# Performance work log

Hardware: AMD Instinct MI355X
Metric: run time of the kernel (lower is better)

Reference implementation:

```python
import jax, jax.numpy as jnp
import numpy as np

NLOC = 10  # local nodes per element (cubic DG triangle)


def setup_inputs() -> dict:
    key = jax.random.key(0)
    ks = jax.random.split(key, 6)
    nele, nloc, ngi = 500000, NLOC, 13
    return {
        "r0": jax.random.normal(ks[0], (nele * nloc,), dtype=jnp.float32),
        "c_i": jax.random.normal(ks[1], (nele * nloc,), dtype=jnp.float32),
        "c_n": jax.random.normal(ks[2], (nele, 1, nloc), dtype=jnp.float32),
        "k": jnp.ones((1,), dtype=jnp.float32),
        "dt": jnp.ones((1,), dtype=jnp.float32),
        "n": jax.random.normal(ks[3], (nloc, ngi), dtype=jnp.float32),
        "nx": jax.random.normal(ks[4], (nele, 2, nloc, ngi), dtype=jnp.float32),
        "detwei": jax.random.uniform(ks[5], (nele, ngi), dtype=jnp.float32),
    }


def reference(r0, c_i, c_n, k, dt, n, nx, detwei):
    nele, _, nloc, ngi = nx.shape
    c_i = c_i.reshape(nele, 1, nloc)               # [e,1,l]
    # stiffness: sum over spatial dims of grad-grad quadrature contraction
    nx1nx1 = jnp.einsum('eig,ejg,eg->eij', nx[:, 0], nx[:, 0], detwei)
    nx2nx2 = jnp.einsum('eig,ejg,eg->eij', nx[:, 1], nx[:, 1], detwei)
    nxnx = (nx1nx1 + nx2nx2) * k                   # [e,i,j] * [1]
    # mass matrix per element (shared shape funcs, per-element detwei)
    nn = jnp.einsum('ig,jg,eg->eij', n, n, detwei)
    # transient branch (config.isTransient = True)
    nn_dt = nn / dt
    nxnx = nn_dt + nxnx
    r0 = r0.reshape(nele, nloc, 1)
    r0 = r0 + jnp.matmul(nn_dt, jnp.swapaxes(c_n, 1, 2))   # [e,i,1]
    r0 = r0.reshape(-1)
    r0 = r0 - jnp.matmul(nxnx, jnp.swapaxes(c_i, 1, 2)).reshape(-1)
    diagA = jnp.diagonal(nxnx, axis1=-2, axis2=-1)          # [e,nloc]
    bdiagA = nxnx
    return (bdiagA, diagA, r0)
```

## Files before the change

### kernel.cpp

```cpp
#include <hip/hip_runtime.h>

#define NLOC  10
#define NGI   13
#define NPAIR 55
#define EPB   32
#define TPB   128

#define B_NX   0
#define B_DW   8320
#define B_R0   8736
#define B_CI   9056
#define B_CN   9376
#define BUF_FL 9696
#define W_N    (2 * BUF_FL)
#define W_TOT  (W_N + 130)

#define GE_NX  2080
#define GE_DW  2184
#define GE_R0  2264
#define GE_CI  2344
#define GE_CN  2424

typedef float vf2 __attribute__((ext_vector_type(2)));

__device__ __forceinline__ constexpr int pidx(int i, int j) {
    return i * NLOC - (i * (i - 1)) / 2 + (j - i);
}

__device__ __forceinline__ void stage16(const float* gsrc, float* lds) {
    __builtin_amdgcn_global_load_lds(
        (const __attribute__((address_space(1))) void*)gsrc,
        (__attribute__((address_space(3))) void*)lds, 16, 0, 0);
}

__global__ __launch_bounds__(TPB, 1) void fem_kernel(
    const float* __restrict__ r0g,
    const float* __restrict__ cig,
    const float* __restrict__ cng,
    const float* __restrict__ kp,
    const float* __restrict__ dtp,
    const float* __restrict__ nmat,
    const float* __restrict__ nx,
    const float* __restrict__ dwei,
    float* __restrict__ out,
    int nele)
{
    __shared__ float sm[W_TOT];

    const int t       = threadIdx.x;
    const int nchunks = (nele + EPB - 1) / EPB;
    const int gs      = gridDim.x;

    auto stage_chunk = [&](int b, int c) {
        const long ce0  = (long)c * EPB;
        const int  crem = min(EPB, nele - (int)ce0);
        const float* snx = nx   + (size_t)ce0 * 260;
        const float* sdw = dwei + (size_t)ce0 * 13;
        const float* sr0 = r0g  + (size_t)ce0 * 10;
        const float* sci = cig  + (size_t)ce0 * 10;
        const float* scn = cng  + (size_t)ce0 * 10;
        const int cnx = crem * 260, cdw = crem * 13, c10 = crem * 10;
        float* ldsb = sm + b * BUF_FL + (t >> 6) * 256;
        #pragma unroll
        for (int k = 0; k < 19; ++k) {
            const int G = k * TPB + t;
            const float* src; int rel, capf;
            if      (G < GE_NX) { src = snx; rel = G;         capf = cnx; }
            else if (G < GE_DW) { src = sdw; rel = G - GE_NX; capf = cdw; }
            else if (G < GE_R0) { src = sr0; rel = G - GE_DW; capf = c10; }
            else if (G < GE_CI) { src = sci; rel = G - GE_R0; capf = c10; }
            else if (G < GE_CN) { src = scn; rel = G - GE_CI; capf = c10; }
            else continue;
            if (rel * 4 < capf) stage16(src + (size_t)rel * 4, ldsb + k * TPB * 4);
        }
    };

    const int  eloc = t >> 2;
    const int  d    = (t >> 1) & 1;
    const int  h    = t & 1;
    const int  q    = t & 3;
    const float kk  = kp[0];
    const float idt = 1.0f / dtp[0];
    const float* smn = sm + W_N;

    int c = blockIdx.x;
    if (c < nchunks) stage_chunk(0, c);
    for (int w = t; w < 130; w += TPB) sm[W_N + w] = nmat[w];
    __syncthreads();

    int cur = 0;
    for (; c < nchunks; c += gs) {
        const int next = c + gs;
        if (next < nchunks) stage_chunk(cur ^ 1, next);

        const long e0   = (long)c * EPB;
        const int  rem  = min(EPB, nele - (int)e0);
        const long e    = e0 + eloc;
        const bool live = eloc < rem;

        const float* bb   = sm + cur * BUF_FL;
        const float* smnx = bb + B_NX + eloc * 260 + d * 130;
        const float* smdw = bb + B_DW + eloc * 13;
        const float* smr0 = bb + B_R0 + eloc * 10;
        const float* smci = bb + B_CI + eloc * 10;
        const float* smcn = bb + B_CN + eloc * 10;

        float civ[NLOC], dif[NLOC];
        #pragma unroll
        for (int l = 0; l < NLOC; ++l) civ[l] = smci[l];
        #pragma unroll
        for (int l = 0; l < NLOC; ++l) dif[l] = smcn[l] - civ[l];

        float acc[NPAIR];
        #pragma unroll
        for (int p = 0; p < NPAIR; ++p) acc[p] = 0.0f;
        float r0a[NLOC];
        #pragma unroll
        for (int i = 0; i < NLOC; ++i) r0a[i] = 0.0f;

        #pragma unroll
        for (int it = 0; it < 7; ++it) {
            const int   graw = 2 * it + h;
            const int   g    = graw < NGI ? graw : NGI - 1;
            const float wv   = graw < NGI ? kk * smdw[g] : 0.0f;
            float col[NLOC];
            #pragma unroll
            for (int l = 0; l < NLOC; ++l) col[l] = smnx[l * 13 + g];
            float u = 0.0f;
            #pragma unroll
            for (int l = 0; l < NLOC; ++l) u = fmaf(col[l], civ[l], u);
            const float uw = u * wv;
            #pragma unroll
            for (int i = 0; i < NLOC; ++i) {
                const float ti = col[i] * wv;
                #pragma unroll
                for (int j = i; j < NLOC; ++j)
                    acc[pidx(i, j)] = fmaf(ti, col[j], acc[pidx(i, j)]);
                r0a[i] = fmaf(-col[i], uw, r0a[i]);
            }
        }

        #pragma unroll
        for (int it = 0; it < 4; ++it) {
            const int   graw = q + 4 * it;
            const int   g    = graw < NGI ? graw : NGI - 1;
            const float wv   = graw < NGI ? idt * smdw[g] : 0.0f;
            float ncol[NLOC];
            #pragma unroll
            for (int l = 0; l < NLOC; ++l) ncol[l] = smn[l * 13 + g];
            float wd = 0.0f;
            #pragma unroll
            for (int l = 0; l < NLOC; ++l) wd = fmaf(ncol[l], dif[l], wd);
            #pragma unroll
            for (int i = 0; i < NLOC; ++i) {
                const float ti = ncol[i] * wv;
                #pragma unroll
                for (int j = i; j < NLOC; ++j)
                    acc[pidx(i, j)] = fmaf(ti, ncol[j], acc[pidx(i, j)]);
                r0a[i] = fmaf(ti, wd, r0a[i]);
            }
        }

        #pragma unroll
        for (int p = 0; p < NPAIR; ++p) {
            acc[p] += __shfl_xor(acc[p], 1);
            acc[p] += __shfl_xor(acc[p], 2);
        }
        #pragma unroll
        for (int i = 0; i < NLOC; ++i) {
            r0a[i] += __shfl_xor(r0a[i], 1);
            r0a[i] += __shfl_xor(r0a[i], 2);
        }

        if (live) {
            float* obd = out + (size_t)e * 100;
            float* odg = out + (size_t)nele * 100 + (size_t)e * 10;
            float* oro = out + (size_t)nele * 110 + (size_t)e * 10;
            #pragma unroll
            for (int i = 0; i < NLOC; ++i) {
                if ((i & 3) == q) {
                    float row[NLOC];
                    #pragma unroll
                    for (int j = 0; j < NLOC; ++j) {
                        const int lo = i < j ? i : j, hi = i < j ? j : i;
                        row[j] = acc[pidx(lo, hi)];
                    }
                    #pragma unroll
                    for (int u2 = 0; u2 < 5; ++u2) {
                        vf2 v = { row[2*u2], row[2*u2+1] };
                        *reinterpret_cast<vf2*>(obd + i * 10 + 2 * u2) = v;
                    }
                    odg[i] = row[i];
                    oro[i] = smr0[i] + r0a[i];
                }
            }
        }

        __syncthreads();
        cur ^= 1;
    }
}

extern "C" void kernel_launch(void* const* d_in, const int* in_sizes, int n_in,
                              void* d_out, int out_size, void* d_ws, size_t ws_size,
                              hipStream_t stream) {
    const float* r0   = (const float*)d_in[0];
    const float* ci   = (const float*)d_in[1];
    const float* cn   = (const float*)d_in[2];
    const float* k    = (const float*)d_in[3];
    const float* dt   = (const float*)d_in[4];
    const float* nmat = (const float*)d_in[5];
    const float* nx   = (const float*)d_in[6];
    const float* dw   = (const float*)d_in[7];
    const int nele = in_sizes[7] / NGI;

    const int nchunks = (nele + EPB - 1) / EPB;
    const int nb = min(512, nchunks);
    fem_kernel<<<nb, TPB, 0, stream>>>(r0, ci, cn, k, dt, nmat, nx, dw,
                                       (float*)d_out, nele);
}
```

Before: 210.7 us.

## Use single-wave blocks, drop barriers, stage outputs in LDS for coalesced stores

Shrinks each block to one 64-thread wave handling 16 elements and doubles the grid. Block-wide barriers are replaced with explicit s_waitcnt vmcnt waits on the asynchronous global-to-LDS loads. Results are first written into the just-consumed LDS buffer, then copied out as contiguous 16-byte nontemporal stores, replacing the scattered 8-byte per-row stores. This relies on single-wave lockstep for LDS ordering, and on vmcnt counting that may be fragile for partial tail chunks.

```diff
diff --git a/kernel.cpp b/kernel.cpp
--- a/kernel.cpp
+++ b/kernel.cpp
@@ -3,25 +3,29 @@
 #define NLOC  10
 #define NGI   13
 #define NPAIR 55
-#define EPB   32
-#define TPB   128
-
-#define B_NX   0
-#define B_DW   8320
-#define B_R0   8736
-#define B_CI   9056
-#define B_CN   9376
-#define BUF_FL 9696
+#define EPB   16
+#define TPB   64
+
+#define B_DW   4160
+#define B_R0   4368
+#define B_CI   4528
+#define B_CN   4688
+#define BUF_FL 4848
 #define W_N    (2 * BUF_FL)
 #define W_TOT  (W_N + 130)
 
-#define GE_NX  2080
-#define GE_DW  2184
-#define GE_R0  2264
-#define GE_CI  2344
-#define GE_CN  2424
+#define GE_NX  1040
+#define GE_DW  1092
+#define GE_R0  1132
+#define GE_CI  1172
+#define GE_CN  1212
+
+#define OS_DG   1600
+#define OS_R0   1760
+#define OS_GRAN 480
 
 typedef float vf2 __attribute__((ext_vector_type(2)));
+typedef float vf4 __attribute__((ext_vector_type(4)));
 
 __device__ __forceinline__ constexpr int pidx(int i, int j) {
     return i * NLOC - (i * (i - 1)) / 2 + (j - i);
@@ -60,7 +64,7 @@
         const float* sci = cig  + (size_t)ce0 * 10;
         const float* scn = cng  + (size_t)ce0 * 10;
         const int cnx = crem * 260, cdw = crem * 13, c10 = crem * 10;
-        float* ldsb = sm + b * BUF_FL + (t >> 6) * 256;
+        float* ldsb = sm + b * BUF_FL;
         #pragma unroll
         for (int k = 0; k < 19; ++k) {
             const int G = k * TPB + t;
@@ -83,23 +87,26 @@
     const float idt = 1.0f / dtp[0];
     const float* smn = sm + W_N;
 
+    for (int w = t; w < 130; w += TPB) sm[W_N + w] = nmat[w];
     int c = blockIdx.x;
     if (c < nchunks) stage_chunk(0, c);
-    for (int w = t; w < 130; w += TPB) sm[W_N + w] = nmat[w];
-    __syncthreads();
 
     int cur = 0;
     for (; c < nchunks; c += gs) {
         const int next = c + gs;
-        if (next < nchunks) stage_chunk(cur ^ 1, next);
+        if (next < nchunks) {
+            stage_chunk(cur ^ 1, next);
+            asm volatile("s_waitcnt vmcnt(19)" ::: "memory");
+        } else {
+            asm volatile("s_waitcnt vmcnt(0)" ::: "memory");
+        }
 
         const long e0   = (long)c * EPB;
         const int  rem  = min(EPB, nele - (int)e0);
-        const long e    = e0 + eloc;
         const bool live = eloc < rem;
 
         const float* bb   = sm + cur * BUF_FL;
-        const float* smnx = bb + B_NX + eloc * 260 + d * 130;
+        const float* smnx = bb + eloc * 260 + d * 130;
         const float* smdw = bb + B_DW + eloc * 13;
         const float* smr0 = bb + B_R0 + eloc * 10;
         const float* smci = bb + B_CI + eloc * 10;
@@ -172,10 +179,8 @@
             r0a[i] += __shfl_xor(r0a[i], 2);
         }
 
+        float* smout = sm + cur * BUF_FL;
         if (live) {
-            float* obd = out + (size_t)e * 100;
-            float* odg = out + (size_t)nele * 100 + (size_t)e * 10;
-            float* oro = out + (size_t)nele * 110 + (size_t)e * 10;
             #pragma unroll
             for (int i = 0; i < NLOC; ++i) {
                 if ((i & 3) == q) {
@@ -188,15 +193,31 @@
                     #pragma unroll
                     for (int u2 = 0; u2 < 5; ++u2) {
                         vf2 v = { row[2*u2], row[2*u2+1] };
-                        *reinterpret_cast<vf2*>(obd + i * 10 + 2 * u2) = v;
+                        *reinterpret_cast<vf2*>(&smout[eloc * 100 + i * 10 + 2 * u2]) = v;
                     }
-                    odg[i] = row[i];
-                    oro[i] = smr0[i] + r0a[i];
+                    smout[OS_DG + eloc * 10 + i] = row[i];
+                    smout[OS_R0 + eloc * 10 + i] = smr0[i] + r0a[i];
                 }
             }
         }
 
-        __syncthreads();
+        const int remg = rem * 30;
+        #pragma unroll
+        for (int k = 0; k < 8; ++k) {
+            const int G = k * TPB + t;
+            if (G < remg && G < OS_GRAN) {
+                vf4 v = *reinterpret_cast<const vf4*>(&smout[G * 4]);
+                float* dst;
+                if (G < 400)
+                    dst = out + (size_t)e0 * 100 + (size_t)G * 4;
+                else if (G < 440)
+                    dst = out + (size_t)nele * 100 + (size_t)e0 * 10 + (size_t)(G - 400) * 4;
+                else
+                    dst = out + (size_t)nele * 110 + (size_t)e0 * 10 + (size_t)(G - 440) * 4;
+                __builtin_nontemporal_store(v, reinterpret_cast<vf4*>(dst));
+            }
+        }
+
         cur ^= 1;
     }
 }
@@ -215,7 +236,7 @@
     const int nele = in_sizes[7] / NGI;
 
     const int nchunks = (nele + EPB - 1) / EPB;
-    const int nb = min(512, nchunks);
+    const int nb = min(1024, nchunks);
     fem_kernel<<<nb, TPB, 0, stream>>>(r0, ci, cn, k, dt, nmat, nx, dw,
                                        (float*)d_out, nele);
 }
```

Result: slower. 221.1 us (+5.0%).
